# Performance work log

Measured on AMD Instinct MI355X. Metric: run time of the kernel, lower is better.

Reference implementation:

```python
import jax, jax.numpy as jnp
import numpy as np

B, S, T, D = 64, 50, 200, 128
IN2, H = 128, 64
NEG = -1e10


def setup_inputs() -> dict:
    key = jax.random.key(0)
    k1, k2, k3, k4, k5, k6, k7, k8 = jax.random.split(key, 8)
    inp = jax.random.normal(k1, (B, S, T, D), dtype=jnp.float32)
    z = jax.random.normal(k2, (B, S, IN2), dtype=jnp.float32)
    mask = jax.random.randint(k3, (B, S, T), 0, 2, dtype=jnp.int32)
    # torch nn.Linear weights: [out, in]
    W1 = jax.random.normal(k4, (H, D), dtype=jnp.float32) / np.sqrt(D)
    W2_w = jax.random.normal(k5, (H, IN2), dtype=jnp.float32) / np.sqrt(IN2)
    W2_b = jax.random.normal(k6, (H,), dtype=jnp.float32) * 0.01
    V_w = jax.random.normal(k7, (1, H), dtype=jnp.float32) / np.sqrt(H)
    V_b = jax.random.normal(k8, (1,), dtype=jnp.float32) * 0.01
    return {"input": inp, "z": z, "mask": mask, "W1": W1,
            "W2_w": W2_w, "W2_b": W2_b, "V_w": V_w, "V_b": V_b}


def reference(input, z, mask, W1, W2_w, W2_b, V_w, V_b):
    # w1h: [B,S,T,H]
    w1h = jnp.einsum('bstd,hd->bsth', input, W1)
    # w2h: [B,S,H] (Linear with bias), broadcast over T
    w2h = jnp.einsum('bsd,hd->bsh', z, W2_w) + W2_b
    u = jnp.tanh(w1h + w2h[:, :, None, :])           # [B,S,T,H]
    att = jnp.einsum('bsth,h->bst', u, V_w[0]) + V_b[0]  # [B,S,T]
    att = jnp.where(mask == 0, NEG, att)
    att = jax.nn.softmax(att, axis=2)
    out = jnp.einsum('bst,bstd->bsd', att, input)    # [B,S,D]
    return out
```

## Files before the change

kernel.cpp:

```cpp
#include <hip/hip_runtime.h>

#define Tdim 200
#define Ddim 128
#define Hdim 64
#define NBS  3200
#define NEGV (-1e10f)

typedef __bf16 bf16x8 __attribute__((ext_vector_type(8)));
typedef float  floatx4 __attribute__((ext_vector_type(4)));

__device__ __forceinline__ unsigned short bf16rne(float f) {
    unsigned int u = __float_as_uint(f);
    u += 0x7fffu + ((u >> 16) & 1u);
    return (unsigned short)(u >> 16);
}

__device__ __forceinline__ float ftanh(float x) {
    float e = __expf(2.0f * x);
    return 1.0f - 2.0f * __builtin_amdgcn_rcpf(e + 1.0f);
}

__global__ void prep(const float* __restrict__ z, const float* __restrict__ W2w,
                     const float* __restrict__ W2b, const float* __restrict__ W1,
                     unsigned short* __restrict__ W1bf, float* __restrict__ w2h) {
    const int tid = threadIdx.x;
    if (blockIdx.x < 800) {
        const int idx = blockIdx.x * 256 + tid;
        const int bs = idx >> 6, h = idx & 63;
        const float* zp = z + bs * 128;
        const float* wp = W2w + h * 128;
        float a = W2b[h];
        #pragma unroll 8
        for (int d = 0; d < 128; ++d) a = fmaf(zp[d], wp[d], a);
        w2h[idx] = a;
    } else {
        const int idx = (blockIdx.x - 800) * 256 + tid;
        const float4* src = (const float4*)W1 + idx * 2;
        float4 v0 = src[0], v1 = src[1];
        uint4 o;
        o.x = bf16rne(v0.x) | ((unsigned int)bf16rne(v0.y) << 16);
        o.y = bf16rne(v0.z) | ((unsigned int)bf16rne(v0.w) << 16);
        o.z = bf16rne(v1.x) | ((unsigned int)bf16rne(v1.y) << 16);
        o.w = bf16rne(v1.z) | ((unsigned int)bf16rne(v1.w) << 16);
        ((uint4*)W1bf)[idx] = o;
    }
}

__global__ __launch_bounds__(256, 3) void attn_main(
    const float* __restrict__ X, const int* __restrict__ mask,
    const float* __restrict__ Vw, const float* __restrict__ Vb,
    const unsigned short* __restrict__ W1bf, const float* __restrict__ w2h_g,
    float* __restrict__ out)
{
    __shared__ __align__(16) unsigned short xs[Tdim * 128];
    __shared__ float attL[Tdim];
    __shared__ float red[8];
    __shared__ float pp[256];

    const int tid = threadIdx.x;
    const int bs  = blockIdx.x;
    const float* __restrict__ Xb = X + (size_t)bs * (Tdim * Ddim);

    #pragma unroll 5
    for (int it = 0; it < 25; ++it) {
        int j = it * 256 + tid;
        int t = j >> 5, dq = j & 31;
        float4 v = *(const float4*)(Xb + t * Ddim + dq * 4);
        unsigned int lo = bf16rne(v.x) | ((unsigned int)bf16rne(v.y) << 16);
        unsigned int hi = bf16rne(v.z) | ((unsigned int)bf16rne(v.w) << 16);
        int u16 = t * 16 + ((dq >> 1) ^ (t & 15));
        *(uint2*)((char*)xs + u16 * 16 + (dq & 1) * 8) = make_uint2(lo, hi);
    }

    const int lane = tid & 63;
    const int wv   = tid >> 6;
    const int l15  = lane & 15, quad = lane >> 4;

    bf16x8 bfrag[4][4];
    #pragma unroll
    for (int n = 0; n < 4; ++n)
        #pragma unroll
        for (int ks = 0; ks < 4; ++ks)
            bfrag[n][ks] = *(const bf16x8*)(W1bf + (n * 16 + l15) * 128 + ks * 32 + quad * 8);

    const float Vb0 = Vb[0];
    float vw[4], w2[4];
    #pragma unroll
    for (int n = 0; n < 4; ++n) {
        int h = l15 + 16 * n;
        vw[n] = Vw[h];
        w2[n] = w2h_g[bs * 64 + h];
    }

    __syncthreads();

    for (int mt = wv; mt < 13; mt += 4) {
        const int t0 = (mt == 12) ? 184 : mt * 16;
        const int trow = t0 + l15;
        floatx4 acc[4];
        #pragma unroll
        for (int n = 0; n < 4; ++n) acc[n] = (floatx4){0.f, 0.f, 0.f, 0.f};
        bf16x8 afrag[4];
        #pragma unroll
        for (int ks = 0; ks < 4; ++ks) {
            int u16 = trow * 16 + (((ks << 2) + quad) ^ (trow & 15));
            afrag[ks] = *(const bf16x8*)(xs + u16 * 8);
        }
        #pragma unroll
        for (int n = 0; n < 4; ++n)
            #pragma unroll
            for (int ks = 0; ks < 4; ++ks)
                acc[n] = __builtin_amdgcn_mfma_f32_16x16x32_bf16(afrag[ks], bfrag[n][ks], acc[n], 0, 0, 0);

        float s0 = 0.f, s1 = 0.f, s2 = 0.f, s3 = 0.f;
        #pragma unroll
        for (int n = 0; n < 4; ++n) {
            s0 = fmaf(ftanh(acc[n][0] + w2[n]), vw[n], s0);
            s1 = fmaf(ftanh(acc[n][1] + w2[n]), vw[n], s1);
            s2 = fmaf(ftanh(acc[n][2] + w2[n]), vw[n], s2);
            s3 = fmaf(ftanh(acc[n][3] + w2[n]), vw[n], s3);
        }
        #pragma unroll
        for (int m = 1; m < 16; m <<= 1) {
            s0 += __shfl_xor(s0, m);
            s1 += __shfl_xor(s1, m);
            s2 += __shfl_xor(s2, m);
            s3 += __shfl_xor(s3, m);
        }
        if (l15 == 0) {
            const int tb = t0 + quad * 4;
            attL[tb]     = s0 + Vb0;
            attL[tb + 1] = s1 + Vb0;
            attL[tb + 2] = s2 + Vb0;
            attL[tb + 3] = s3 + Vb0;
        }
    }
    __syncthreads();

    float l = -3e38f;
    if (tid < Tdim) {
        l = attL[tid];
        if (mask[bs * Tdim + tid] == 0) l = NEGV;
    }
    float m = l;
    #pragma unroll
    for (int off = 32; off > 0; off >>= 1) m = fmaxf(m, __shfl_xor(m, off));
    if (lane == 0) red[wv] = m;
    __syncthreads();
    const float M = fmaxf(fmaxf(red[0], red[1]), fmaxf(red[2], red[3]));
    float p = __expf(l - M);
    float sm = p;
    #pragma unroll
    for (int off = 32; off > 0; off >>= 1) sm += __shfl_xor(sm, off);
    if (lane == 0) red[4 + wv] = sm;
    __syncthreads();
    const float S = (red[4] + red[5]) + (red[6] + red[7]);
    if (tid < Tdim) attL[tid] = p / S;
    __syncthreads();

    const int d = tid & 127, half = tid >> 7;
    const float* xp = Xb + half * 100 * Ddim + d;
    float o = 0.f;
    #pragma unroll 4
    for (int tt = 0; tt < 100; ++tt)
        o = fmaf(attL[half * 100 + tt], xp[tt * Ddim], o);
    pp[tid] = o;
    __syncthreads();
    if (tid < 128) out[bs * Ddim + tid] = pp[tid] + pp[tid + 128];
}

extern "C" void kernel_launch(void* const* d_in, const int* in_sizes, int n_in,
                              void* d_out, int out_size, void* d_ws, size_t ws_size,
                              hipStream_t stream) {
    const float* X    = (const float*)d_in[0];
    const float* z    = (const float*)d_in[1];
    const int*   mask = (const int*)d_in[2];
    const float* W1   = (const float*)d_in[3];
    const float* W2w  = (const float*)d_in[4];
    const float* W2b  = (const float*)d_in[5];
    const float* Vw   = (const float*)d_in[6];
    const float* Vb   = (const float*)d_in[7];
    float* out = (float*)d_out;

    unsigned short* W1bf = (unsigned short*)d_ws;
    float* w2h = (float*)((char*)d_ws + 16384);

    prep<<<804, 256, 0, stream>>>(z, W2w, W2b, W1, W1bf, w2h);
    attn_main<<<NBS, 256, 0, stream>>>(X, mask, Vw, Vb, W1bf, w2h, out);
}
```

Before: 502.4 us.

## Fuse prep into main kernel, switch to fp16 MFMA, reuse LDS tile for weighted sum

Removes the separate prep kernel: each block now converts its W1 fragments to fp16 itself and computes its own w2h row (z·W2^T+b) into shared memory. The MFMA path switches from bf16 to fp16. The final attention-weighted sum over T now reads the fp16 copy of X already held in LDS instead of re-reading fp32 X from global memory. This saves a kernel launch and a second pass over X, but adds redundant per-block W1 conversion and W2 work, and uses fp16 input values in the output sum, which lowers precision.

```diff
diff --git a/kernel.cpp b/kernel.cpp
--- a/kernel.cpp
+++ b/kernel.cpp
@@ -6,13 +6,13 @@
 #define NBS  3200
 #define NEGV (-1e10f)
 
-typedef __bf16 bf16x8 __attribute__((ext_vector_type(8)));
-typedef float  floatx4 __attribute__((ext_vector_type(4)));
+typedef _Float16 f16x8 __attribute__((ext_vector_type(8)));
+typedef float    floatx4 __attribute__((ext_vector_type(4)));
 
-__device__ __forceinline__ unsigned short bf16rne(float f) {
-    unsigned int u = __float_as_uint(f);
-    u += 0x7fffu + ((u >> 16) & 1u);
-    return (unsigned short)(u >> 16);
+__device__ __forceinline__ unsigned int packf16(float a, float b) {
+    _Float16 ha = (_Float16)a, hb = (_Float16)b;
+    unsigned int ua = *(unsigned short*)&ha, ub = *(unsigned short*)&hb;
+    return ua | (ub << 16);
 }
 
 __device__ __forceinline__ float ftanh(float x) {
@@ -20,42 +20,19 @@
     return 1.0f - 2.0f * __builtin_amdgcn_rcpf(e + 1.0f);
 }
 
-__global__ void prep(const float* __restrict__ z, const float* __restrict__ W2w,
-                     const float* __restrict__ W2b, const float* __restrict__ W1,
-                     unsigned short* __restrict__ W1bf, float* __restrict__ w2h) {
-    const int tid = threadIdx.x;
-    if (blockIdx.x < 800) {
-        const int idx = blockIdx.x * 256 + tid;
-        const int bs = idx >> 6, h = idx & 63;
-        const float* zp = z + bs * 128;
-        const float* wp = W2w + h * 128;
-        float a = W2b[h];
-        #pragma unroll 8
-        for (int d = 0; d < 128; ++d) a = fmaf(zp[d], wp[d], a);
-        w2h[idx] = a;
-    } else {
-        const int idx = (blockIdx.x - 800) * 256 + tid;
-        const float4* src = (const float4*)W1 + idx * 2;
-        float4 v0 = src[0], v1 = src[1];
-        uint4 o;
-        o.x = bf16rne(v0.x) | ((unsigned int)bf16rne(v0.y) << 16);
-        o.y = bf16rne(v0.z) | ((unsigned int)bf16rne(v0.w) << 16);
-        o.z = bf16rne(v1.x) | ((unsigned int)bf16rne(v1.y) << 16);
-        o.w = bf16rne(v1.z) | ((unsigned int)bf16rne(v1.w) << 16);
-        ((uint4*)W1bf)[idx] = o;
-    }
-}
-
 __global__ __launch_bounds__(256, 3) void attn_main(
-    const float* __restrict__ X, const int* __restrict__ mask,
+    const float* __restrict__ X, const float* __restrict__ z,
+    const int* __restrict__ mask,
+    const float* __restrict__ W1, const float* __restrict__ W2w,
+    const float* __restrict__ W2b,
     const float* __restrict__ Vw, const float* __restrict__ Vb,
-    const unsigned short* __restrict__ W1bf, const float* __restrict__ w2h_g,
     float* __restrict__ out)
 {
     __shared__ __align__(16) unsigned short xs[Tdim * 128];
     __shared__ float attL[Tdim];
     __shared__ float red[8];
     __shared__ float pp[256];
+    __shared__ float w2hL[Hdim];
 
     const int tid = threadIdx.x;
     const int bs  = blockIdx.x;
@@ -66,8 +43,8 @@
         int j = it * 256 + tid;
         int t = j >> 5, dq = j & 31;
         float4 v = *(const float4*)(Xb + t * Ddim + dq * 4);
-        unsigned int lo = bf16rne(v.x) | ((unsigned int)bf16rne(v.y) << 16);
-        unsigned int hi = bf16rne(v.z) | ((unsigned int)bf16rne(v.w) << 16);
+        unsigned int lo = packf16(v.x, v.y);
+        unsigned int hi = packf16(v.z, v.w);
         int u16 = t * 16 + ((dq >> 1) ^ (t & 15));
         *(uint2*)((char*)xs + u16 * 16 + (dq & 1) * 8) = make_uint2(lo, hi);
     }
@@ -76,23 +53,45 @@
     const int wv   = tid >> 6;
     const int l15  = lane & 15, quad = lane >> 4;
 
-    bf16x8 bfrag[4][4];
+    f16x8 bfrag[4][4];
     #pragma unroll
     for (int n = 0; n < 4; ++n)
         #pragma unroll
-        for (int ks = 0; ks < 4; ++ks)
-            bfrag[n][ks] = *(const bf16x8*)(W1bf + (n * 16 + l15) * 128 + ks * 32 + quad * 8);
+        for (int ks = 0; ks < 4; ++ks) {
+            const float* wp = W1 + (n * 16 + l15) * 128 + ks * 32 + quad * 8;
+            float4 v0 = *(const float4*)wp;
+            float4 v1 = *(const float4*)(wp + 4);
+            uint4 u = make_uint4(packf16(v0.x, v0.y), packf16(v0.z, v0.w),
+                                 packf16(v1.x, v1.y), packf16(v1.z, v1.w));
+            bfrag[n][ks] = *(f16x8*)&u;
+        }
+
+    {
+        const int h = tid >> 2, q = tid & 3;
+        const float4* zp = (const float4*)(z + (size_t)bs * 128 + q * 32);
+        const float4* wp = (const float4*)(W2w + h * 128 + q * 32);
+        float a = 0.f;
+        #pragma unroll
+        for (int i = 0; i < 8; ++i) {
+            float4 zv = zp[i], wv4 = wp[i];
+            a = fmaf(zv.x, wv4.x, a); a = fmaf(zv.y, wv4.y, a);
+            a = fmaf(zv.z, wv4.z, a); a = fmaf(zv.w, wv4.w, a);
+        }
+        a += __shfl_xor(a, 1);
+        a += __shfl_xor(a, 2);
+        if (q == 0) w2hL[h] = a + W2b[h];
+    }
 
     const float Vb0 = Vb[0];
-    float vw[4], w2[4];
+    float vw[4];
     #pragma unroll
-    for (int n = 0; n < 4; ++n) {
-        int h = l15 + 16 * n;
-        vw[n] = Vw[h];
-        w2[n] = w2h_g[bs * 64 + h];
-    }
+    for (int n = 0; n < 4; ++n) vw[n] = Vw[l15 + 16 * n];
 
     __syncthreads();
+
+    float w2[4];
+    #pragma unroll
+    for (int n = 0; n < 4; ++n) w2[n] = w2hL[l15 + 16 * n];
 
     for (int mt = wv; mt < 13; mt += 4) {
         const int t0 = (mt == 12) ? 184 : mt * 16;
@@ -100,17 +99,17 @@
         floatx4 acc[4];
         #pragma unroll
         for (int n = 0; n < 4; ++n) acc[n] = (floatx4){0.f, 0.f, 0.f, 0.f};
-        bf16x8 afrag[4];
+        f16x8 afrag[4];
         #pragma unroll
         for (int ks = 0; ks < 4; ++ks) {
             int u16 = trow * 16 + (((ks << 2) + quad) ^ (trow & 15));
-            afrag[ks] = *(const bf16x8*)(xs + u16 * 8);
+            afrag[ks] = *(const f16x8*)(xs + u16 * 8);
         }
         #pragma unroll
         for (int n = 0; n < 4; ++n)
             #pragma unroll
             for (int ks = 0; ks < 4; ++ks)
-                acc[n] = __builtin_amdgcn_mfma_f32_16x16x32_bf16(afrag[ks], bfrag[n][ks], acc[n], 0, 0, 0);
+                acc[n] = __builtin_amdgcn_mfma_f32_16x16x32_f16(afrag[ks], bfrag[n][ks], acc[n], 0, 0, 0);
 
         float s0 = 0.f, s1 = 0.f, s2 = 0.f, s3 = 0.f;
         #pragma unroll
@@ -159,11 +158,15 @@
     __syncthreads();
 
     const int d = tid & 127, half = tid >> 7;
-    const float* xp = Xb + half * 100 * Ddim + d;
+    const _Float16* xsh = (const _Float16*)xs;
+    const int d3 = d >> 3, dl = d & 7;
     float o = 0.f;
     #pragma unroll 4
-    for (int tt = 0; tt < 100; ++tt)
-        o = fmaf(attL[half * 100 + tt], xp[tt * Ddim], o);
+    for (int tt = 0; tt < 100; ++tt) {
+        int t = half * 100 + tt;
+        int idx = t * 128 + ((d3 ^ (t & 15)) << 3) + dl;
+        o = fmaf(attL[t], (float)xsh[idx], o);
+    }
     pp[tid] = o;
     __syncthreads();
     if (tid < 128) out[bs * Ddim + tid] = pp[tid] + pp[tid + 128];
@@ -182,9 +185,5 @@
     const float* Vb   = (const float*)d_in[7];
     float* out = (float*)d_out;
 
-    unsigned short* W1bf = (unsigned short*)d_ws;
-    float* w2h = (float*)((char*)d_ws + 16384);
-
-    prep<<<804, 256, 0, stream>>>(z, W2w, W2b, W1, W1bf, w2h);
-    attn_main<<<NBS, 256, 0, stream>>>(X, mask, Vw, Vb, W1bf, w2h, out);
+    attn_main<<<NBS, 256, 0, stream>>>(X, z, mask, W1, W2w, W2b, Vw, Vb, out);
 }
```

Result: faster. 490.3 us (-2.4%).
